# Optimization experiments

Hardware: AMD Instinct MI355X
Metric: run time of the kernel (lower is better)

The kernel has to match this reference:

```python
import jax, jax.numpy as jnp
import numpy as np

N, F_IN, H, O = 8192, 512, 256, 64


def setup_inputs() -> dict:
    key = jax.random.key(0)
    ks = jax.random.split(key, 7)
    scale = 1.0 / np.sqrt(N)  # keep N x N matmul chain numerically tame
    x = jax.random.normal(ks[0], (N, F_IN), dtype=jnp.float32)
    wavelets = jax.random.normal(ks[1], (N, N), dtype=jnp.float32) * scale
    wavelets_inv = jax.random.normal(ks[2], (N, N), dtype=jnp.float32) * scale
    w1 = jax.random.normal(ks[3], (F_IN, H), dtype=jnp.float32) * (1.0 / np.sqrt(F_IN))
    f1 = jax.random.uniform(ks[4], (N,), dtype=jnp.float32, minval=0.9, maxval=1.1)
    w2 = jax.random.normal(ks[5], (H, O), dtype=jnp.float32) * (1.0 / np.sqrt(H))
    f2 = jax.random.uniform(ks[6], (N,), dtype=jnp.float32, minval=0.9, maxval=1.1)
    return {"x": x, "wavelets": wavelets, "wavelets_inv": wavelets_inv,
            "w1": w1, "f1": f1, "w2": w2, "f2": f2}


def _gwnn_layer(feat, wavelets, wavelets_inv, w, filt):
    # Original: wavelets @ diag(filt) @ (wavelets_inv @ (feat @ w)).
    # diag(filt) @ M is a row-scale: same math, O(N*d) instead of O(N^3).
    t = feat @ w                      # [N, d_out]
    t = wavelets_inv @ t              # [N, d_out]
    return wavelets @ (filt[:, None] * t)


def reference(x, wavelets, wavelets_inv, w1, f1, w2, f2):
    h = jax.nn.relu(_gwnn_layer(x, wavelets, wavelets_inv, w1, f1))
    # dropout is identity in eval mode
    o = _gwnn_layer(h, wavelets, wavelets_inv, w2, f2)
    return jax.nn.log_softmax(o, axis=1)
```

## Files before the change

kernel.cpp:

```cpp
#include <hip/hip_runtime.h>
#include <hip/hip_bf16.h>
#include <cstdint>
#include <cstddef>

typedef __attribute__((ext_vector_type(8))) __bf16 bf16x8;
typedef __attribute__((ext_vector_type(8))) unsigned short ushort8;
typedef __attribute__((ext_vector_type(4))) float f32x4;

#define DEVINL __device__ __forceinline__

DEVINL unsigned short f2bf(float f) {
    union { float f; unsigned int i; } v; v.f = f;
    unsigned int u = v.i;
    unsigned int r = (u + 0x7fffu + ((u >> 16) & 1u)) >> 16;
    return (unsigned short)r;
}

template<int BM, int BN, int EPI, bool AF32>
__global__ __launch_bounds__(256)
void gemm_bt(const void* __restrict__ Av, const short* __restrict__ Bt,
             void* __restrict__ Cv, const float* __restrict__ fvec,
             int M, int K, int Ncols)
{
    constexpr int BK = 64;
    constexpr int WTM = BM / 2;
    constexpr int WTN = BN / 2;
    constexpr int FM = WTM / 16;
    constexpr int FN = WTN / 16;
    constexpr int CA = (BM * 8) / 256;
    constexpr int CB = (BN * 8) / 256;

    __shared__ __align__(16) short smem[(BM + BN) * BK];
    short* smA = smem;
    short* smB = smem + BM * BK;

    const int t  = threadIdx.x;
    const int m0 = blockIdx.x * BM;
    const int n0 = blockIdx.y * BN;

    const int w    = t >> 6;
    const int lane = t & 63;
    const int wm   = w >> 1;
    const int wn   = w & 1;
    const int lr   = lane & 15;
    const int q    = lane >> 4;

    f32x4 acc[FM][FN];
#pragma unroll
    for (int i = 0; i < FM; ++i)
#pragma unroll
        for (int j = 0; j < FN; ++j)
            acc[i][j] = f32x4{0.f, 0.f, 0.f, 0.f};

    int aoff[FM][2], boff[FN][2];
#pragma unroll
    for (int i = 0; i < FM; ++i) {
        int row = wm * WTM + i * 16 + lr;
#pragma unroll
        for (int s = 0; s < 2; ++s)
            aoff[i][s] = row * BK + (((s * 4 + q) ^ (row & 7)) * 8);
    }
#pragma unroll
    for (int j = 0; j < FN; ++j) {
        int row = wn * WTN + j * 16 + lr;
#pragma unroll
        for (int s = 0; s < 2; ++s)
            boff[j][s] = row * BK + (((s * 4 + q) ^ (row & 7)) * 8);
    }

    const float* aSrcF[CA]; const short* aSrcH[CA]; short* aDst[CA];
#pragma unroll
    for (int i = 0; i < CA; ++i) {
        int c = i * 256 + t;
        int row = c >> 3;
        int gc = (c & 7) ^ (row & 7);
        size_t eoff = (size_t)(m0 + row) * K + gc * 8;
        if constexpr (AF32) aSrcF[i] = (const float*)Av + eoff;
        else                aSrcH[i] = (const short*)Av + eoff;
        aDst[i] = smA + c * 8;
    }
    const short* bSrc[CB]; short* bDst[CB];
#pragma unroll
    for (int i = 0; i < CB; ++i) {
        int c = i * 256 + t;
        int row = c >> 3;
        int gc = (c & 7) ^ (row & 7);
        bSrc[i] = Bt + (size_t)(n0 + row) * K + gc * 8;
        bDst[i] = smB + c * 8;
    }

    for (int k0 = 0; k0 < K; k0 += BK) {
        ushort8 ra[CA], rb[CB];
#pragma unroll
        for (int i = 0; i < CA; ++i) {
            if constexpr (AF32) {
                f32x4 lo = *(const f32x4*)(const void*)(aSrcF[i] + k0);
                f32x4 hi = *(const f32x4*)(const void*)(aSrcF[i] + k0 + 4);
                ushort8 r;
                r[0] = f2bf(lo[0]); r[1] = f2bf(lo[1]); r[2] = f2bf(lo[2]); r[3] = f2bf(lo[3]);
                r[4] = f2bf(hi[0]); r[5] = f2bf(hi[1]); r[6] = f2bf(hi[2]); r[7] = f2bf(hi[3]);
                ra[i] = r;
            } else {
                ra[i] = *(const ushort8*)(const void*)(aSrcH[i] + k0);
            }
        }
#pragma unroll
        for (int i = 0; i < CB; ++i) rb[i] = *(const ushort8*)(const void*)(bSrc[i] + k0);

        __syncthreads();
#pragma unroll
        for (int i = 0; i < CA; ++i) *(ushort8*)(void*)aDst[i] = ra[i];
#pragma unroll
        for (int i = 0; i < CB; ++i) *(ushort8*)(void*)bDst[i] = rb[i];
        __syncthreads();

#pragma unroll
        for (int s = 0; s < 2; ++s) {
            bf16x8 fa[FM], fb[FN];
#pragma unroll
            for (int i = 0; i < FM; ++i)
                fa[i] = *(const bf16x8*)(const void*)(smA + aoff[i][s]);
#pragma unroll
            for (int j = 0; j < FN; ++j)
                fb[j] = *(const bf16x8*)(const void*)(smB + boff[j][s]);
#pragma unroll
            for (int i = 0; i < FM; ++i)
#pragma unroll
                for (int j = 0; j < FN; ++j)
                    acc[i][j] = __builtin_amdgcn_mfma_f32_16x16x32_bf16(
                        fa[i], fb[j], acc[i][j], 0, 0, 0);
        }
    }

#pragma unroll
    for (int i = 0; i < FM; ++i) {
        const int m_base = m0 + wm * WTM + i * 16 + q * 4;
        float s0 = 1.f, s1 = 1.f, s2 = 1.f, s3 = 1.f;
        if constexpr (EPI == 1) {
            s0 = fvec[m_base + 0];
            s1 = fvec[m_base + 1];
            s2 = fvec[m_base + 2];
            s3 = fvec[m_base + 3];
        }
#pragma unroll
        for (int j = 0; j < FN; ++j) {
            const int n_g = n0 + wn * WTN + j * 16 + lr;
            f32x4 v = acc[i][j];
            if constexpr (EPI == 0 || EPI == 1) {
                ushort4 o4;
                o4.x = f2bf(v[0] * s0);
                o4.y = f2bf(v[1] * s1);
                o4.z = f2bf(v[2] * s2);
                o4.w = f2bf(v[3] * s3);
                *(ushort4*)((unsigned short*)Cv + (size_t)n_g * M + m_base) = o4;
            } else if constexpr (EPI == 2) {
                unsigned short* Cp = (unsigned short*)Cv;
#pragma unroll
                for (int r = 0; r < 4; ++r) {
                    float val = v[r];
                    val = val > 0.f ? val : 0.f;
                    Cp[(size_t)(m_base + r) * Ncols + n_g] = f2bf(val);
                }
            } else {
                *(f32x4*)((float*)Cv + (size_t)n_g * M + m_base) = v;
            }
        }
    }
}

__global__ __launch_bounds__(256)
void transpose_f32_to_bf16(const float* __restrict__ in,
                           unsigned short* __restrict__ out, int R, int C)
{
    int idx = blockIdx.x * 256 + threadIdx.x;
    if (idx < R * C) {
        int r = idx / C, c = idx - r * C;
        out[(size_t)c * R + r] = f2bf(in[idx]);
    }
}

__global__ __launch_bounds__(256)
void logsoftmax64(const float* __restrict__ oT, float* __restrict__ out, int M)
{
    int m = blockIdx.x * 256 + threadIdx.x;
    float mx = -1e30f;
    for (int j = 0; j < 64; ++j) mx = fmaxf(mx, oT[(size_t)j * M + m]);
    float s = 0.f;
    for (int j = 0; j < 64; ++j) s += __expf(oT[(size_t)j * M + m] - mx);
    float ls = mx + __logf(s);
    for (int j = 0; j < 64; ++j)
        out[(size_t)m * 64 + j] = oT[(size_t)j * M + m] - ls;
}

extern "C" void kernel_launch(void* const* d_in, const int* in_sizes, int n_in,
                              void* d_out, int out_size, void* d_ws, size_t ws_size,
                              hipStream_t stream)
{
    constexpr int N = 8192, FIN = 512, H = 256, O = 64;
    const float* x    = (const float*)d_in[0];
    const float* wav  = (const float*)d_in[1];
    const float* winv = (const float*)d_in[2];
    const float* w1   = (const float*)d_in[3];
    const float* f1   = (const float*)d_in[4];
    const float* w2   = (const float*)d_in[5];
    const float* f2   = (const float*)d_in[6];

    char* p = (char*)d_ws;
    auto alloc = [&](size_t bytes) { char* r = p; p += (bytes + 255) & ~(size_t)255; return r; };
    short* w1T = (short*)alloc((size_t)FIN * H * 2);
    short* w2T = (short*)alloc((size_t)H * O * 2);
    short* t1T = (short*)alloc((size_t)H * N * 2);
    short* t2T = (short*)alloc((size_t)H * N * 2);
    short* hbuf= (short*)alloc((size_t)N * H * 2);
    short* t4T = (short*)alloc((size_t)O * N * 2);
    short* t5T = (short*)alloc((size_t)O * N * 2);
    float* oT  = (float*)alloc((size_t)O * N * 4);

    transpose_f32_to_bf16<<<(FIN * H + 255) / 256, 256, 0, stream>>>(
        w1, (unsigned short*)w1T, FIN, H);
    transpose_f32_to_bf16<<<(H * O + 255) / 256, 256, 0, stream>>>(
        w2, (unsigned short*)w2T, H, O);

    gemm_bt<64,128,0,true><<<dim3(N/64, H/128), 256, 0, stream>>>(x, w1T, t1T, nullptr, N, FIN, H);
    gemm_bt<64,128,1,true><<<dim3(N/64, H/128), 256, 0, stream>>>(winv, t1T, t2T, f1, N, N, H);
    gemm_bt<64,128,2,true><<<dim3(N/64, H/128), 256, 0, stream>>>(wav, t2T, hbuf, nullptr, N, N, H);
    gemm_bt<64,64,0,false><<<dim3(N/64, O/64), 256, 0, stream>>>(hbuf, w2T, t4T, nullptr, N, H, O);
    gemm_bt<32,64,1,true><<<dim3(N/32, O/64), 256, 0, stream>>>(winv, t4T, t5T, f2, N, N, O);
    gemm_bt<32,64,3,true><<<dim3(N/32, O/64), 256, 0, stream>>>(wav, t5T, oT, nullptr, N, N, O);
    logsoftmax64<<<N / 256, 256, 0, stream>>>(oT, (float*)d_out, N);
}
```

Before: 1.006 ms.

## Split-K the large N×N GEMMs and fuse epilogues into reduction kernels

The four large N×N GEMMs now split the K dimension across blockIdx.z (4 splits for the H=256 layer, 8 for the O=64 layer). Each split writes fp32 partial sums, and new reduction kernels apply the filter scaling, the ReLU with a transpose, or the log-softmax. Previously these GEMMs launched only 256 or 256 blocks, which underfills the GPU; the split multiplies block count to raise occupancy. The cost is extra fp32 partial traffic (up to 4×256×8192 floats), additional kernel launches, and a small change in fp32 summation order.

```diff
diff --git a/kernel.cpp b/kernel.cpp
--- a/kernel.cpp
+++ b/kernel.cpp
@@ -16,7 +16,7 @@
     return (unsigned short)r;
 }
 
-template<int BM, int BN, int EPI, bool AF32>
+template<int BM, int BN, int EPI, bool AF32, int KS>
 __global__ __launch_bounds__(256)
 void gemm_bt(const void* __restrict__ Av, const short* __restrict__ Bt,
              void* __restrict__ Cv, const float* __restrict__ fvec,
@@ -37,6 +37,10 @@
     const int t  = threadIdx.x;
     const int m0 = blockIdx.x * BM;
     const int n0 = blockIdx.y * BN;
+    const int z  = (KS > 1) ? blockIdx.z : 0;
+    const int Kc = K / KS;
+    const int kbeg = z * Kc;
+    const int kend = kbeg + Kc;
 
     const int w    = t >> 6;
     const int lane = t & 63;
@@ -89,7 +93,7 @@
         bDst[i] = smB + c * 8;
     }
 
-    for (int k0 = 0; k0 < K; k0 += BK) {
+    for (int k0 = kbeg; k0 < kend; k0 += BK) {
         ushort8 ra[CA], rb[CB];
 #pragma unroll
         for (int i = 0; i < CA; ++i) {
@@ -136,7 +140,7 @@
     for (int i = 0; i < FM; ++i) {
         const int m_base = m0 + wm * WTM + i * 16 + q * 4;
         float s0 = 1.f, s1 = 1.f, s2 = 1.f, s3 = 1.f;
-        if constexpr (EPI == 1) {
+        if constexpr (EPI == 1 && KS == 1) {
             s0 = fvec[m_base + 0];
             s1 = fvec[m_base + 1];
             s2 = fvec[m_base + 2];
@@ -146,23 +150,16 @@
         for (int j = 0; j < FN; ++j) {
             const int n_g = n0 + wn * WTN + j * 16 + lr;
             f32x4 v = acc[i][j];
-            if constexpr (EPI == 0 || EPI == 1) {
+            if constexpr (KS > 1) {
+                float* P = (float*)Cv + (size_t)z * Ncols * M;
+                *(f32x4*)(P + (size_t)n_g * M + m_base) = v;
+            } else if constexpr (EPI == 0 || EPI == 1) {
                 ushort4 o4;
                 o4.x = f2bf(v[0] * s0);
                 o4.y = f2bf(v[1] * s1);
                 o4.z = f2bf(v[2] * s2);
                 o4.w = f2bf(v[3] * s3);
                 *(ushort4*)((unsigned short*)Cv + (size_t)n_g * M + m_base) = o4;
-            } else if constexpr (EPI == 2) {
-                unsigned short* Cp = (unsigned short*)Cv;
-#pragma unroll
-                for (int r = 0; r < 4; ++r) {
-                    float val = v[r];
-                    val = val > 0.f ? val : 0.f;
-                    Cp[(size_t)(m_base + r) * Ncols + n_g] = f2bf(val);
-                }
-            } else {
-                *(f32x4*)((float*)Cv + (size_t)n_g * M + m_base) = v;
             }
         }
     }
@@ -179,17 +176,91 @@
     }
 }
 
+template<int KS, bool SCALE>
 __global__ __launch_bounds__(256)
-void logsoftmax64(const float* __restrict__ oT, float* __restrict__ out, int M)
-{
-    int m = blockIdx.x * 256 + threadIdx.x;
+void reduce_scaleT(const float* __restrict__ p, unsigned short* __restrict__ out,
+                   const float* __restrict__ fvec, size_t zs)
+{
+    size_t base = ((size_t)blockIdx.x * 256 + threadIdx.x) * 4;
+    f32x4 s = *(const f32x4*)(p + base);
+#pragma unroll
+    for (int zz = 1; zz < KS; ++zz)
+        s += *(const f32x4*)(p + (size_t)zz * zs + base);
+    if constexpr (SCALE) {
+        const int m = (int)(base & 8191);
+        f32x4 f = *(const f32x4*)(fvec + m);
+        s[0] *= f[0]; s[1] *= f[1]; s[2] *= f[2]; s[3] *= f[3];
+    }
+    ushort4 o4;
+    o4.x = f2bf(s[0]); o4.y = f2bf(s[1]); o4.z = f2bf(s[2]); o4.w = f2bf(s[3]);
+    *(ushort4*)(out + base) = o4;
+}
+
+template<int KS>
+__global__ __launch_bounds__(256)
+void reduce_relu_trans(const float* __restrict__ p, unsigned short* __restrict__ out,
+                       int M, int H)
+{
+    __shared__ float tile[64][65];
+    const int t  = threadIdx.x;
+    const int m0 = blockIdx.x * 64;
+    const int n0 = blockIdx.y * 64;
+    const size_t zs = (size_t)H * M;
+#pragma unroll
+    for (int pass = 0; pass < 4; ++pass) {
+        int n  = pass * 16 + (t >> 4);
+        int mo = (t & 15) * 4;
+        const float* src = p + (size_t)(n0 + n) * M + (m0 + mo);
+        f32x4 s = *(const f32x4*)src;
+#pragma unroll
+        for (int zz = 1; zz < KS; ++zz)
+            s += *(const f32x4*)(src + (size_t)zz * zs);
+        tile[mo + 0][n] = fmaxf(s[0], 0.f);
+        tile[mo + 1][n] = fmaxf(s[1], 0.f);
+        tile[mo + 2][n] = fmaxf(s[2], 0.f);
+        tile[mo + 3][n] = fmaxf(s[3], 0.f);
+    }
+    __syncthreads();
+#pragma unroll
+    for (int pass = 0; pass < 4; ++pass) {
+        int mm = pass * 16 + (t >> 4);
+        int c  = (t & 15) * 4;
+        ushort4 o4;
+        o4.x = f2bf(tile[mm][c + 0]);
+        o4.y = f2bf(tile[mm][c + 1]);
+        o4.z = f2bf(tile[mm][c + 2]);
+        o4.w = f2bf(tile[mm][c + 3]);
+        *(ushort4*)(out + (size_t)(m0 + mm) * H + (n0 + c)) = o4;
+    }
+}
+
+template<int KS>
+__global__ __launch_bounds__(64)
+void reduce_lsm(const float* __restrict__ p, float* __restrict__ out, int M)
+{
+    int m = blockIdx.x * 64 + threadIdx.x;
+    const size_t zs = (size_t)64 * M;
+    float v[64];
+#pragma unroll
+    for (int j = 0; j < 64; ++j) {
+        const float* src = p + (size_t)j * M + m;
+        float s = src[0];
+#pragma unroll
+        for (int zz = 1; zz < KS; ++zz) s += src[(size_t)zz * zs];
+        v[j] = s;
+    }
     float mx = -1e30f;
-    for (int j = 0; j < 64; ++j) mx = fmaxf(mx, oT[(size_t)j * M + m]);
-    float s = 0.f;
-    for (int j = 0; j < 64; ++j) s += __expf(oT[(size_t)j * M + m] - mx);
-    float ls = mx + __logf(s);
-    for (int j = 0; j < 64; ++j)
-        out[(size_t)m * 64 + j] = oT[(size_t)j * M + m] - ls;
+#pragma unroll
+    for (int j = 0; j < 64; ++j) mx = fmaxf(mx, v[j]);
+    float sum = 0.f;
+#pragma unroll
+    for (int j = 0; j < 64; ++j) sum += __expf(v[j] - mx);
+    float ls = mx + __logf(sum);
+#pragma unroll
+    for (int j = 0; j < 64; j += 4) {
+        f32x4 o = {v[j] - ls, v[j + 1] - ls, v[j + 2] - ls, v[j + 3] - ls};
+        *(f32x4*)(out + (size_t)m * 64 + j) = o;
+    }
 }
 
 extern "C" void kernel_launch(void* const* d_in, const int* in_sizes, int n_in,
@@ -197,6 +268,8 @@
                               hipStream_t stream)
 {
     constexpr int N = 8192, FIN = 512, H = 256, O = 64;
+    constexpr int KS_H = 4;
+    constexpr int KS_O = 8;
     const float* x    = (const float*)d_in[0];
     const float* wav  = (const float*)d_in[1];
     const float* winv = (const float*)d_in[2];
@@ -214,18 +287,35 @@
     short* hbuf= (short*)alloc((size_t)N * H * 2);
     short* t4T = (short*)alloc((size_t)O * N * 2);
     short* t5T = (short*)alloc((size_t)O * N * 2);
-    float* oT  = (float*)alloc((size_t)O * N * 4);
+    float* part= (float*)alloc((size_t)KS_H * H * N * 4);
 
     transpose_f32_to_bf16<<<(FIN * H + 255) / 256, 256, 0, stream>>>(
         w1, (unsigned short*)w1T, FIN, H);
     transpose_f32_to_bf16<<<(H * O + 255) / 256, 256, 0, stream>>>(
         w2, (unsigned short*)w2T, H, O);
 
-    gemm_bt<64,128,0,true><<<dim3(N/64, H/128), 256, 0, stream>>>(x, w1T, t1T, nullptr, N, FIN, H);
-    gemm_bt<64,128,1,true><<<dim3(N/64, H/128), 256, 0, stream>>>(winv, t1T, t2T, f1, N, N, H);
-    gemm_bt<64,128,2,true><<<dim3(N/64, H/128), 256, 0, stream>>>(wav, t2T, hbuf, nullptr, N, N, H);
-    gemm_bt<64,64,0,false><<<dim3(N/64, O/64), 256, 0, stream>>>(hbuf, w2T, t4T, nullptr, N, H, O);
-    gemm_bt<32,64,1,true><<<dim3(N/32, O/64), 256, 0, stream>>>(winv, t4T, t5T, f2, N, N, O);
-    gemm_bt<32,64,3,true><<<dim3(N/32, O/64), 256, 0, stream>>>(wav, t5T, oT, nullptr, N, N, O);
-    logsoftmax64<<<N / 256, 256, 0, stream>>>(oT, (float*)d_out, N);
-}
+    gemm_bt<64,128,0,true,1><<<dim3(N/64, H/128), 256, 0, stream>>>(
+        x, w1T, t1T, nullptr, N, FIN, H);
+
+    gemm_bt<64,128,0,true,KS_H><<<dim3(N/64, H/128, KS_H), 256, 0, stream>>>(
+        winv, t1T, part, nullptr, N, N, H);
+    reduce_scaleT<KS_H,true><<<(H * (N / 4)) / 256, 256, 0, stream>>>(
+        part, (unsigned short*)t2T, f1, (size_t)H * N);
+
+    gemm_bt<64,128,0,true,KS_H><<<dim3(N/64, H/128, KS_H), 256, 0, stream>>>(
+        wav, t2T, part, nullptr, N, N, H);
+    reduce_relu_trans<KS_H><<<dim3(N/64, H/64), 256, 0, stream>>>(
+        part, (unsigned short*)hbuf, N, H);
+
+    gemm_bt<32,64,0,false,1><<<dim3(N/32, O/64), 256, 0, stream>>>(
+        hbuf, w2T, t4T, nullptr, N, H, O);
+
+    gemm_bt<32,64,0,true,KS_O><<<dim3(N/32, O/64, KS_O), 256, 0, stream>>>(
+        winv, t4T, part, nullptr, N, N, O);
+    reduce_scaleT<KS_O,true><<<(O * (N / 4)) / 256, 256, 0, stream>>>(
+        part, (unsigned short*)t5T, f2, (size_t)O * N);
+
+    gemm_bt<32,64,0,true,KS_O><<<dim3(N/32, O/64, KS_O), 256, 0, stream>>>(
+        wav, t5T, part, nullptr, N, N, O);
+    reduce_lsm<KS_O><<<N / 64, 64, 0, stream>>>(part, (float*)d_out, N);
+}
```

New measurement: 854.4 us. 15.1% less time.
